# Optimization experiments

Measured on AMD Instinct MI355X. Metric: run time of the kernel, lower is better.

The kernel has to match this reference:

```python
import jax, jax.numpy as jnp
import numpy as np

D, H, M, FF = 1024, 16, 64, 4096
B, N, C = 8, 1024, 256


def setup_inputs() -> dict:
    key = jax.random.key(0)
    it = iter(jax.random.split(key, 24))
    def nrm(shape, s):
        return jax.random.normal(next(it), shape, dtype=jnp.float32) * s
    z = lambda *s: jnp.zeros(s, jnp.float32)
    inp = {
        'point_tokens': nrm((B, N, D), 1.0),
        'context_tokens': nrm((B, C, D), 1.0),
        'inducing': nrm((1, M, D), 0.02),
    }
    for p in ('ti', 'tp'):  # to_induced / to_points MHA
        for w in ('Wq', 'Wk', 'Wv', 'Wo'):
            inp[f'{p}_{w}'] = nrm((D, D), 0.02)
        for b in ('bq', 'bk', 'bv', 'bo'):
            inp[f'{p}_{b}'] = z(D)
    for p in ('iff', 'pff'):  # induced_ff / point_ff: LN + Linear + GELU + Linear
        inp[f'{p}_g'] = jnp.ones(D, jnp.float32); inp[f'{p}_b'] = z(D)
        inp[f'{p}_W1'] = nrm((D, FF), 0.02); inp[f'{p}_b1'] = z(FF)
        inp[f'{p}_W2'] = nrm((FF, D), 0.02); inp[f'{p}_b2'] = z(D)
    inp['ni_g'] = jnp.ones(D, jnp.float32); inp['ni_b'] = z(D)
    inp['np_g'] = jnp.ones(D, jnp.float32); inp['np_b'] = z(D)
    return inp


def layernorm(x, g, b, eps=1e-5):
    mu = x.mean(-1, keepdims=True)
    var = ((x - mu) ** 2).mean(-1, keepdims=True)
    return (x - mu) * jax.lax.rsqrt(var + eps) * g + b


def ffn(x, g, b0, W1, b1, W2, b2):
    h = layernorm(x, g, b0)
    h = jax.nn.gelu(h @ W1 + b1, approximate=False)  # torch nn.GELU default = exact erf
    return h @ W2 + b2


def mha(q, kv, Wq, bq, Wk, bk, Wv, bv, Wo, bo):
    # torch nn.MultiheadAttention semantics (batch_first, dropout=0, need_weights=True)
    Bq, Lq, Dm = q.shape
    Lk = kv.shape[1]
    hd = Dm // H
    Q = (q @ Wq + bq).reshape(Bq, Lq, H, hd)
    K = (kv @ Wk + bk).reshape(Bq, Lk, H, hd)
    V = (kv @ Wv + bv).reshape(Bq, Lk, H, hd)
    scores = jnp.einsum('bqhd,bkhd->bhqk', Q, K) / jnp.sqrt(jnp.float32(hd))
    probs = jax.nn.softmax(scores, axis=-1)
    out = jnp.einsum('bhqk,bkhd->bqhd', probs, V).reshape(Bq, Lq, Dm)
    return out @ Wo + bo, probs.mean(axis=1)  # head-averaged weights (need_weights default)


def reference(point_tokens, context_tokens, inducing,
              ti_Wq, ti_bq, ti_Wk, ti_bk, ti_Wv, ti_bv, ti_Wo, ti_bo,
              tp_Wq, tp_bq, tp_Wk, tp_bk, tp_Wv, tp_bv, tp_Wo, tp_bo,
              iff_g, iff_b, iff_W1, iff_b1, iff_W2, iff_b2,
              pff_g, pff_b, pff_W1, pff_b1, pff_W2, pff_b2,
              ni_g, ni_b, np_g, np_b):
    b = point_tokens.shape[0]
    induced = jnp.broadcast_to(inducing, (b, inducing.shape[1], inducing.shape[2]))
    kv = jnp.concatenate([context_tokens, point_tokens], axis=1)
    ia, _ = mha(induced, kv, ti_Wq, ti_bq, ti_Wk, ti_bk, ti_Wv, ti_bv, ti_Wo, ti_bo)
    induced = layernorm(induced + ia, ni_g, ni_b)
    induced = induced + ffn(induced, iff_g, iff_b, iff_W1, iff_b1, iff_W2, iff_b2)
    kv2 = jnp.concatenate([context_tokens, induced], axis=1)
    pa, w2 = mha(point_tokens, kv2, tp_Wq, tp_bq, tp_Wk, tp_bk, tp_Wv, tp_bv, tp_Wo, tp_bo)
    pts = layernorm(point_tokens + pa, np_g, np_b)
    pts = pts + ffn(pts, pff_g, pff_b, pff_W1, pff_b1, pff_W2, pff_b2)
    probs = jnp.clip(w2, 1e-8, None)
    entropy = (-(probs * jnp.log(probs)).sum(axis=-1)).mean()  # detached side output
    return pts, entropy
```

## Files before the change

kernel.cpp:

```cpp
#include <hip/hip_runtime.h>
#include <hip/hip_bf16.h>
#include <math.h>

typedef unsigned short ushort_t;
typedef __attribute__((ext_vector_type(8))) short short8;
typedef __attribute__((ext_vector_type(4))) float f32x4;

static __device__ __forceinline__ ushort_t f2b(float f){
  union{float f;unsigned u;}a; a.f=f;
  unsigned r = a.u + 0x7fffu + ((a.u>>16)&1u);
  return (ushort_t)(r>>16);
}
static __device__ __forceinline__ float b2f(ushort_t u){
  union{unsigned u;float f;}a; a.u=((unsigned)u)<<16; return a.f;
}

#define GLDS16(g,l) __builtin_amdgcn_global_load_lds((const __attribute__((address_space(1))) void*)(const void*)(g), (__attribute__((address_space(3))) void*)(void*)(l), 16, 0, 0)

template<bool GELU, int RES>
__global__ __launch_bounds__(256)
void gemm_bt(const ushort_t* __restrict__ A, const ushort_t* __restrict__ Bt,
             const float* __restrict__ bias, const void* __restrict__ Res,
             float* __restrict__ Cf, ushort_t* __restrict__ Cb,
             int M, int N, int K, int lda, int ldb, int ldres, int ldcf, int ldcb,
             int nb0,
             long sA0, long sA1, long sB0, long sB1, long sR0, long sR1,
             long sCf0, long sCf1, long sCb0, long sCb1, float scale, int resMask)
{
  const int z = blockIdx.z;
  const int b0 = z % nb0, b1 = z / nb0;
  A  += b0*sA0 + b1*sA1;
  Bt += b0*sB0 + b1*sB1;
  const float* RpF = 0; const ushort_t* RpB = 0;
  if (RES==1) RpF = (const float*)Res + b0*sR0 + b1*sR1;
  if (RES==2) RpB = (const ushort_t*)Res + b0*sR0 + b1*sR1;
  if (Cf) Cf += b0*sCf0 + b1*sCf1;
  if (Cb) Cb += b0*sCb0 + b1*sCb1;

  const int gx = gridDim.x;
  const int nwg = gx * gridDim.y;
  const int orig = blockIdx.y*gx + blockIdx.x;
  const int q8 = nwg >> 3, r8 = nwg & 7;
  const int xcd = orig & 7, ii = orig >> 3;
  const int wg = (xcd < r8 ? xcd*(q8+1) : r8*(q8+1) + (xcd-r8)*q8) + ii;
  const int bm = (wg / gx)*128, bn = (wg % gx)*128;

  __shared__ __align__(16) ushort_t As[2][4096];
  __shared__ __align__(16) ushort_t Bs[2][4096];
  const int tid = threadIdx.x, lane = tid&63, wave = tid>>6;
  const int wr = wave>>1, wc = wave&1;

  f32x4 acc[4][4] = {};

  const int c0 = wave*64 + lane;
  const int c1 = c0 + 256;
  const long rA0 = min(bm + (c0>>2), M-1);
  const long rA1 = min(bm + (c1>>2), M-1);
  const long rB0 = min(bn + (c0>>2), N-1);
  const long rB1 = min(bn + (c1>>2), N-1);
  const ushort_t* pA0 = A + rA0*lda + (c0&3)*8;
  const ushort_t* pA1 = A + rA1*lda + (c1&3)*8;
  const ushort_t* pB0 = Bt + rB0*ldb + (c0&3)*8;
  const ushort_t* pB1 = Bt + rB1*ldb + (c1&3)*8;
  const int ldsOff = wave*512;

  const int lr = lane&15, lk = (lane>>4)*8;

#define STAGE(buf, kt) do { \
    GLDS16(pA0 + (kt), &As[buf][ldsOff]); \
    GLDS16(pA1 + (kt), &As[buf][2048 + ldsOff]); \
    GLDS16(pB0 + (kt), &Bs[buf][ldsOff]); \
    GLDS16(pB1 + (kt), &Bs[buf][2048 + ldsOff]); \
  } while(0)

  STAGE(0, 0);
  __syncthreads();
  int cur = 0;
  for (int kt = 0; kt < K; kt += 32) {
    if (kt + 32 < K) STAGE(cur^1, kt+32);
    short8 af[4], bfv[4];
#pragma unroll
    for (int m=0;m<4;m++) af[m]  = *(const short8*)(&As[cur][(wr*64+m*16+lr)*32 + lk]);
#pragma unroll
    for (int n=0;n<4;n++) bfv[n] = *(const short8*)(&Bs[cur][(wc*64+n*16+lr)*32 + lk]);
#pragma unroll
    for (int m=0;m<4;m++)
#pragma unroll
      for (int n=0;n<4;n++)
        acc[m][n] = __builtin_amdgcn_mfma_f32_16x16x32_bf16(af[m], bfv[n], acc[m][n], 0, 0, 0);
    __syncthreads();
    cur ^= 1;
  }
#undef STAGE

  const int orow = bm + wr*64, ocol = bn + wc*64;
  const int rsub = (lane>>4)*4;
#pragma unroll
  for (int n=0;n<4;n++){
    const int col = ocol + n*16 + lr;
    if (col >= N) continue;
    const float bv = bias ? bias[col] : 0.f;
#pragma unroll
    for (int m=0;m<4;m++){
#pragma unroll
      for (int i=0;i<4;i++){
        const int row = orow + m*16 + rsub + i;
        if (row >= M) continue;
        float v = acc[m][n][i]*scale + bv;
        if (GELU) v = 0.5f*v*(1.f + erff(v*0.70710678118654752f));
        if (RES==1) v += RpF[(long)(row & resMask)*ldres + col];
        if (RES==2) v += b2f(RpB[(long)(row & resMask)*ldres + col]);
        if (Cf) Cf[(long)row*ldcf + col] = v;
        if (Cb) Cb[(long)row*ldcb + col] = f2b(v);
      }
    }
  }
}

template<bool WRITEP>
__global__ __launch_bounds__(256)
void fattn_k(const ushort_t* __restrict__ Qb, const ushort_t* __restrict__ KVb,
             const ushort_t* __restrict__ Vtb, ushort_t* __restrict__ Ob,
             ushort_t* __restrict__ Pb,
             int LK, int ldkv, int qRowsPerB, int oRowsPerB, float scale)
{
  const int z = blockIdx.z, b = z >> 4, h = z & 15;
  const int qt = blockIdx.x;
  const int tid = threadIdx.x, lane = tid & 63, wave = tid >> 6;
  const int lr = lane & 15, g = lane >> 4;

  __shared__ __align__(16) ushort_t Kls[64*68];
  __shared__ __align__(16) ushort_t Vtls[64*68];
  __shared__ __align__(16) ushort_t Pls[64*68];

  const long qrow = (long)b*qRowsPerB + qt*64 + wave*16 + lr;
  const short8 aq0 = *(const short8*)(Qb + qrow*1024 + h*64 + g*8);
  const short8 aq1 = *(const short8*)(Qb + qrow*1024 + h*64 + 32 + g*8);

  const ushort_t* Kbase = KVb + (long)b*LK*ldkv + h*64;
  const ushort_t* Vtbase = Vtb + (long)(b*16+h)*64*LK;

  const int ntiles = LK >> 6;
  const int r0 = tid>>3, d0c = (tid&7)*8;
  const int r1 = r0 + 32;

  float m[4] = {-3e30f,-3e30f,-3e30f,-3e30f};
  float l[4] = {0.f,0.f,0.f,0.f};

  for (int t=0; t<ntiles; ++t){
    __syncthreads();
    { short8 v0 = *(const short8*)(Kbase + (long)(t*64 + r0)*ldkv + d0c);
      short8 v1 = *(const short8*)(Kbase + (long)(t*64 + r1)*ldkv + d0c);
      *(short8*)(Kls + r0*68 + d0c) = v0;
      *(short8*)(Kls + r1*68 + d0c) = v1; }
    __syncthreads();
    f32x4 s[4];
#pragma unroll
    for(int n=0;n<4;n++){
      s[n] = (f32x4){0.f,0.f,0.f,0.f};
      short8 bk0 = *(const short8*)(Kls + (n*16+lr)*68 + g*8);
      short8 bk1 = *(const short8*)(Kls + (n*16+lr)*68 + 32 + g*8);
      s[n] = __builtin_amdgcn_mfma_f32_16x16x32_bf16(aq0, bk0, s[n],0,0,0);
      s[n] = __builtin_amdgcn_mfma_f32_16x16x32_bf16(aq1, bk1, s[n],0,0,0);
    }
#pragma unroll
    for(int i=0;i<4;i++){
      float mx = fmaxf(fmaxf(s[0][i],s[1][i]), fmaxf(s[2][i],s[3][i])) * scale;
#pragma unroll
      for(int o2=1;o2<16;o2<<=1) mx = fmaxf(mx, __shfl_xor(mx,o2));
      float mnew = fmaxf(m[i], mx);
      float sum = __expf(s[0][i]*scale-mnew)+__expf(s[1][i]*scale-mnew)
                + __expf(s[2][i]*scale-mnew)+__expf(s[3][i]*scale-mnew);
#pragma unroll
      for(int o2=1;o2<16;o2<<=1) sum += __shfl_xor(sum,o2);
      l[i] = l[i]*__expf(m[i]-mnew) + sum;
      m[i] = mnew;
    }
  }
  float invl[4];
#pragma unroll
  for(int i=0;i<4;i++) invl[i] = 1.f/l[i];

  f32x4 o[4];
#pragma unroll
  for(int n=0;n<4;n++) o[n] = (f32x4){0.f,0.f,0.f,0.f};

  long pbase = 0;
  if (WRITEP) pbase = ((long)(b*16+h)*1024 + qt*64 + wave*16)*320 + lr;

  for (int t=0; t<ntiles; ++t){
    __syncthreads();
    { short8 v0 = *(const short8*)(Kbase + (long)(t*64 + r0)*ldkv + d0c);
      short8 v1 = *(const short8*)(Kbase + (long)(t*64 + r1)*ldkv + d0c);
      short8 w0 = *(const short8*)(Vtbase + (long)r0*LK + t*64 + d0c);
      short8 w1 = *(const short8*)(Vtbase + (long)r1*LK + t*64 + d0c);
      *(short8*)(Kls + r0*68 + d0c) = v0;
      *(short8*)(Kls + r1*68 + d0c) = v1;
      *(short8*)(Vtls + r0*68 + d0c) = w0;
      *(short8*)(Vtls + r1*68 + d0c) = w1; }
    __syncthreads();
    f32x4 s[4];
#pragma unroll
    for(int n=0;n<4;n++){
      s[n] = (f32x4){0.f,0.f,0.f,0.f};
      short8 bk0 = *(const short8*)(Kls + (n*16+lr)*68 + g*8);
      short8 bk1 = *(const short8*)(Kls + (n*16+lr)*68 + 32 + g*8);
      s[n] = __builtin_amdgcn_mfma_f32_16x16x32_bf16(aq0, bk0, s[n],0,0,0);
      s[n] = __builtin_amdgcn_mfma_f32_16x16x32_bf16(aq1, bk1, s[n],0,0,0);
    }
#pragma unroll
    for(int n=0;n<4;n++){
#pragma unroll
      for(int i=0;i<4;i++){
        float e = __expf(s[n][i]*scale - m[i]);
        Pls[(wave*16 + g*4 + i)*68 + n*16 + lr] = f2b(e);
        if (WRITEP) Pb[pbase + (long)(g*4+i)*320 + t*64 + n*16] = f2b(e*invl[i]);
      }
    }
    short8 pa0 = *(const short8*)(Pls + (wave*16+lr)*68 + g*8);
    short8 pa1 = *(const short8*)(Pls + (wave*16+lr)*68 + 32 + g*8);
#pragma unroll
    for(int nd=0; nd<4; nd++){
      short8 vb0 = *(const short8*)(Vtls + (nd*16+lr)*68 + g*8);
      short8 vb1 = *(const short8*)(Vtls + (nd*16+lr)*68 + 32 + g*8);
      o[nd] = __builtin_amdgcn_mfma_f32_16x16x32_bf16(pa0, vb0, o[nd],0,0,0);
      o[nd] = __builtin_amdgcn_mfma_f32_16x16x32_bf16(pa1, vb1, o[nd],0,0,0);
    }
  }
  const long orow0 = (long)b*oRowsPerB + qt*64 + wave*16 + g*4;
#pragma unroll
  for(int nd=0;nd<4;nd++)
#pragma unroll
    for(int i=0;i<4;i++)
      Ob[(orow0+i)*1024 + h*64 + nd*16 + lr] = f2b(o[nd][i]*invl[i]);
}

__global__ __launch_bounds__(256)
void tcvt_k(const float* __restrict__ src, ushort_t* __restrict__ dst, int R, int C)
{
  __shared__ float t[32][33];
  int c0 = blockIdx.x*32, r0 = blockIdx.y*32;
  int tx = threadIdx.x & 31, ty = threadIdx.x >> 5;
  for (int i=ty;i<32;i+=8){ int r=r0+i, c=c0+tx; t[i][tx] = (r<R && c<C) ? src[(long)r*C + c] : 0.f; }
  __syncthreads();
  for (int i=ty;i<32;i+=8){ int c=c0+i, r=r0+tx; if (c<C && r<R) dst[(long)c*R + r] = f2b(t[tx][i]); }
}

__global__ __launch_bounds__(256)
void cvt_rows_k(const float* __restrict__ src, ushort_t* __restrict__ dst,
                long total, int R, long dstBS, long dstRO)
{
  long e = ((long)blockIdx.x*256 + threadIdx.x)*4;
  if (e >= total) return;
  long rc = e >> 10; int c = (int)(e & 1023);
  int r = (int)(rc % R); long b = rc / R;
  float4 v = *(const float4*)(src + e);
  ushort4 o; o.x=f2b(v.x); o.y=f2b(v.y); o.z=f2b(v.z); o.w=f2b(v.w);
  *(ushort4*)(dst + (b*dstBS + dstRO + r)*1024 + c) = o;
}

__global__ __launch_bounds__(256)
void vtrans_k(const ushort_t* __restrict__ V, ushort_t* __restrict__ Vt,
              int Lk, int ldv, int coloff)
{
  int b = blockIdx.z, h = blockIdx.y, k0 = blockIdx.x*32;
  __shared__ ushort_t t[32][65];
  int tx = threadIdx.x & 63, ty = threadIdx.x >> 6;
  for (int i=ty;i<32;i+=4) t[i][tx] = V[((long)b*Lk + k0 + i)*ldv + coloff + h*64 + tx];
  __syncthreads();
  int kk = threadIdx.x & 31, n0 = threadIdx.x >> 5;
  for (int n=n0;n<64;n+=8) Vt[((long)(b*16+h)*64 + n)*Lk + k0 + kk] = t[kk][n];
}

__global__ __launch_bounds__(256)
void ln2x_k(const float* __restrict__ x,
            const float* __restrict__ g1, const float* __restrict__ b1,
            const float* __restrict__ g2, const float* __restrict__ b2,
            float* __restrict__ y1f, ushort_t* __restrict__ y1b, ushort_t* __restrict__ y2b)
{
  const long row = blockIdx.x;
  int tid = threadIdx.x, lane = tid&63, wave = tid>>6;
  __shared__ float red[8], red2[8];
  float4 v = ((const float4*)(x + row*1024))[tid];
  float s = v.x+v.y+v.z+v.w;
  for (int o=32;o;o>>=1) s += __shfl_down(s,o);
  if (lane==0) red[wave]=s;
  __syncthreads();
  float mean = (red[0]+red[1]+red[2]+red[3])*(1.f/1024.f);
  float d0=v.x-mean, d1=v.y-mean, d2=v.z-mean, d3=v.w-mean;
  float q = d0*d0+d1*d1+d2*d2+d3*d3;
  for (int o=32;o;o>>=1) q += __shfl_down(q,o);
  if (lane==0) red[4+wave]=q;
  __syncthreads();
  float var = (red[4]+red[5]+red[6]+red[7])*(1.f/1024.f);
  float rs = rsqrtf(var+1e-5f);
  float4 gg=((const float4*)g1)[tid], bb=((const float4*)b1)[tid];
  float y0=d0*rs*gg.x+bb.x, y1v=d1*rs*gg.y+bb.y, y2v=d2*rs*gg.z+bb.z, y3=d3*rs*gg.w+bb.w;
  if (y1f) ((float4*)(y1f+row*1024))[tid] = make_float4(y0,y1v,y2v,y3);
  if (y1b){ ushort4 o4; o4.x=f2b(y0); o4.y=f2b(y1v); o4.z=f2b(y2v); o4.w=f2b(y3);
            ((ushort4*)(y1b+row*1024))[tid]=o4; }
  float s2 = y0+y1v+y2v+y3;
  for (int o=32;o;o>>=1) s2 += __shfl_down(s2,o);
  if (lane==0) red2[wave]=s2;
  __syncthreads();
  float mean2 = (red2[0]+red2[1]+red2[2]+red2[3])*(1.f/1024.f);
  float e0=y0-mean2,e1=y1v-mean2,e2=y2v-mean2,e3=y3-mean2;
  float q2 = e0*e0+e1*e1+e2*e2+e3*e3;
  for (int o=32;o;o>>=1) q2 += __shfl_down(q2,o);
  if (lane==0) red2[4+wave]=q2;
  __syncthreads();
  float var2 = (red2[4]+red2[5]+red2[6]+red2[7])*(1.f/1024.f);
  float rs2 = rsqrtf(var2+1e-5f);
  float4 g2v=((const float4*)g2)[tid], b2v=((const float4*)b2)[tid];
  ushort4 o4;
  o4.x=f2b(e0*rs2*g2v.x+b2v.x); o4.y=f2b(e1*rs2*g2v.y+b2v.y);
  o4.z=f2b(e2*rs2*g2v.z+b2v.z); o4.w=f2b(e3*rs2*g2v.w+b2v.w);
  ((ushort4*)(y2b+row*1024))[tid]=o4;
}

__global__ __launch_bounds__(256)
void w2ent_k(const ushort_t* __restrict__ P, float* __restrict__ rowent)
{
  int wid = (int)((blockIdx.x*256 + threadIdx.x) >> 6);
  int lane = threadIdx.x & 63;
  int b = wid >> 10, q = wid & 1023;
  const ushort_t* base = P + ((long)(b*16)*1024 + q)*320;
  float acc = 0.f;
#pragma unroll
  for (int j=0;j<5;j++){
    int k = j*64 + lane;
    float s = 0.f;
#pragma unroll
    for (int h=0;h<16;h++) s += b2f(base[(long)h*327680 + k]);
    float p = fmaxf(s*(1.f/16.f), 1e-8f);
    acc += p*__logf(p);
  }
  for (int o=32;o;o>>=1) acc += __shfl_down(acc, o);
  if (lane==0) rowent[wid] = acc;
}

__global__ __launch_bounds__(256)
void entfin_k(const float* __restrict__ rowent, float* __restrict__ out)
{
  float s = 0.f;
  for (int i=threadIdx.x;i<8192;i+=256) s += rowent[i];
  __shared__ float red[4];
  for (int o=32;o;o>>=1) s += __shfl_down(s,o);
  if ((threadIdx.x&63)==0) red[threadIdx.x>>6]=s;
  __syncthreads();
  if (threadIdx.x==0) out[0] = -(red[0]+red[1]+red[2]+red[3]) * (1.f/8192.f);
}

__global__ void dbg_k(float* out, float a){ out[0] = -12345.f; out[1] = a; }

static void gemm(hipStream_t s, int mode,
                 const void* A, const void* Bt, const float* bias, const void* Res,
                 void* Cf, void* Cb,
                 int M, int N, int K, int lda, int ldb, int ldres, int ldcf, int ldcb,
                 int nz, int nb0,
                 long sA0, long sA1, long sB0, long sB1, long sR0, long sR1,
                 long sCf0, long sCf1, long sCb0, long sCb1, float scale, int resMask)
{
  dim3 g((N+127)/128, (M+127)/128, nz), b(256,1,1);
#define ARGS (const ushort_t*)A,(const ushort_t*)Bt,bias,Res,(float*)Cf,(ushort_t*)Cb,M,N,K,lda,ldb,ldres,ldcf,ldcb,nb0,sA0,sA1,sB0,sB1,sR0,sR1,sCf0,sCf1,sCb0,sCb1,scale,resMask
  if      (mode == 1) gemm_bt<true ,0><<<g,b,0,s>>>(ARGS);
  else if (mode == 2) gemm_bt<false,1><<<g,b,0,s>>>(ARGS);
  else if (mode == 3) gemm_bt<false,2><<<g,b,0,s>>>(ARGS);
  else                gemm_bt<false,0><<<g,b,0,s>>>(ARGS);
#undef ARGS
}

extern "C" void kernel_launch(void* const* d_in, const int* in_sizes, int n_in,
                              void* d_out, int out_size, void* d_ws, size_t ws_size,
                              hipStream_t stream)
{
  const float* ptsIn = (const float*)d_in[0];
  const float* ctx   = (const float*)d_in[1];
  const float* induc = (const float*)d_in[2];
  const float* tiW[4]={(const float*)d_in[3],(const float*)d_in[4],(const float*)d_in[5],(const float*)d_in[6]};
  const float* tib[4]={(const float*)d_in[7],(const float*)d_in[8],(const float*)d_in[9],(const float*)d_in[10]};
  const float* tpW[4]={(const float*)d_in[11],(const float*)d_in[12],(const float*)d_in[13],(const float*)d_in[14]};
  const float* tpb[4]={(const float*)d_in[15],(const float*)d_in[16],(const float*)d_in[17],(const float*)d_in[18]};
  const float* iff_g=(const float*)d_in[19]; const float* iff_b=(const float*)d_in[20];
  const float* iffW1=(const float*)d_in[21]; const float* iff_b1=(const float*)d_in[22];
  const float* iffW2=(const float*)d_in[23]; const float* iff_b2=(const float*)d_in[24];
  const float* pff_g=(const float*)d_in[25]; const float* pff_b=(const float*)d_in[26];
  const float* pffW1=(const float*)d_in[27]; const float* pff_b1=(const float*)d_in[28];
  const float* pffW2=(const float*)d_in[29]; const float* pff_b2=(const float*)d_in[30];
  const float* ni_g=(const float*)d_in[31]; const float* ni_b=(const float*)d_in[32];
  const float* np_g=(const float*)d_in[33]; const float* np_b=(const float*)d_in[34];
  float* outF = (float*)d_out;

  char* ws = (char*)d_ws;
  size_t off = 0;
  auto alloc = [&](size_t bytes){ off=(off+255)&~(size_t)255; size_t o=off; off+=bytes; return o; };
  auto sub = [&](size_t& pp, size_t bytes){ pp=(pp+255)&~(size_t)255; size_t o=pp; pp+=bytes; return o; };

  size_t o_tiQw  = alloc(1024L*1024*2);
  size_t o_tiKVw = alloc(2048L*1024*2);
  size_t o_tiOw  = alloc(1024L*1024*2);
  size_t o_tpQw  = alloc(1024L*1024*2);
  size_t o_tpKVw = alloc(2048L*1024*2);
  size_t o_tpOw  = alloc(1024L*1024*2);
  size_t o_iffW1t = alloc(4096L*1024*2);
  size_t o_iffW2t = alloc(4096L*1024*2);
  size_t o_pffW1t = alloc(4096L*1024*2);
  size_t o_pffW2t = alloc(4096L*1024*2);
  size_t o_bti  = alloc(2048*4);
  size_t o_btp  = alloc(2048*4);
  size_t o_indb = alloc(64L*1024*2);
  size_t o_kv   = alloc(10240L*1024*2);
  size_t o_kv2  = alloc(2560L*1024*2);
  size_t o_rowent = alloc(8192*4);
  off=(off+255)&~(size_t)255;
  size_t arena = off;

  size_t p = arena;
  size_t o_Qti     = sub(p, 64L*1024*2);
  size_t o_KVti    = sub(p, 10240L*2048*2);
  size_t o_Vtti    = sub(p, 8192L*1280*2);
  size_t o_attnOti = sub(p, 512L*1024*2);
  size_t o_t1      = sub(p, 512L*1024*4);
  size_t o_ind1    = sub(p, 512L*1024*4);
  size_t o_h0i     = sub(p, 512L*1024*2);
  size_t o_h1i     = sub(p, 512L*4096*2);
  size_t need1 = p;
  p = arena;
  size_t o_attnOtp = sub(p, 8192L*1024*2);
  size_t shared = p;
  size_t o_Qtp  = sub(p, 8192L*1024*2);
  size_t o_KVtp = sub(p, 2560L*2048*2);
  size_t o_Vttp = sub(p, 8192L*320*2);
  size_t o_P    = sub(p, 8L*16*1024*320*2);
  size_t need3 = p;
  p = shared;
  size_t o_t2   = sub(p, 8192L*1024*4);
  size_t o_pts1 = sub(p, 8192L*1024*2);
  size_t o_h0p  = sub(p, 8192L*1024*2);
  size_t o_h1p  = sub(p, 8192L*4096*2);
  size_t need4 = p;

  size_t need = need1;
  if (need3>need) need=need3;
  if (need4>need) need=need4;
  if (need > ws_size){ dbg_k<<<1,1,0,stream>>>(outF, (float)(need>>20)); return; }

#define WP(o) ((void*)(ws + (o)))
#define BP(o) ((ushort_t*)(ws + (o)))
#define FP(o) ((float*)(ws + (o)))
  const long Z0[10] = {0,0,0,0,0,0,0,0,0,0};

  tcvt_k<<<dim3(32,32),256,0,stream>>>(tiW[0], BP(o_tiQw), 1024, 1024);
  tcvt_k<<<dim3(32,32),256,0,stream>>>(tiW[1], BP(o_tiKVw), 1024, 1024);
  tcvt_k<<<dim3(32,32),256,0,stream>>>(tiW[2], BP(o_tiKVw) + 1024L*1024, 1024, 1024);
  tcvt_k<<<dim3(32,32),256,0,stream>>>(tiW[3], BP(o_tiOw), 1024, 1024);
  tcvt_k<<<dim3(32,32),256,0,stream>>>(tpW[0], BP(o_tpQw), 1024, 1024);
  tcvt_k<<<dim3(32,32),256,0,stream>>>(tpW[1], BP(o_tpKVw), 1024, 1024);
  tcvt_k<<<dim3(32,32),256,0,stream>>>(tpW[2], BP(o_tpKVw) + 1024L*1024, 1024, 1024);
  tcvt_k<<<dim3(32,32),256,0,stream>>>(tpW[3], BP(o_tpOw), 1024, 1024);
  tcvt_k<<<dim3(128,32),256,0,stream>>>(iffW1, BP(o_iffW1t), 1024, 4096);
  tcvt_k<<<dim3(32,128),256,0,stream>>>(iffW2, BP(o_iffW2t), 4096, 1024);
  tcvt_k<<<dim3(128,32),256,0,stream>>>(pffW1, BP(o_pffW1t), 1024, 4096);
  tcvt_k<<<dim3(32,128),256,0,stream>>>(pffW2, BP(o_pffW2t), 4096, 1024);
  hipMemcpyAsync(WP(o_bti), (const void*)tib[1], 1024*4, hipMemcpyDeviceToDevice, stream);
  hipMemcpyAsync((void*)(ws+o_bti+1024*4), (const void*)tib[2], 1024*4, hipMemcpyDeviceToDevice, stream);
  hipMemcpyAsync(WP(o_btp), (const void*)tpb[1], 1024*4, hipMemcpyDeviceToDevice, stream);
  hipMemcpyAsync((void*)(ws+o_btp+1024*4), (const void*)tpb[2], 1024*4, hipMemcpyDeviceToDevice, stream);

  cvt_rows_k<<<2048,256,0,stream>>>(ctx,   BP(o_kv),  8L*256*1024, 256, 1280, 0);
  cvt_rows_k<<<8192,256,0,stream>>>(ptsIn, BP(o_kv),  8L*1024*1024, 1024, 1280, 256);
  cvt_rows_k<<<64,256,0,stream>>>(induc,   BP(o_indb), 64L*1024, 64, 64, 0);
  cvt_rows_k<<<2048,256,0,stream>>>(ctx,   BP(o_kv2), 8L*256*1024, 256, 320, 0);

  gemm(stream,0, WP(o_indb), WP(o_tiQw), tib[0], 0, 0, WP(o_Qti),
       64,1024,1024, 1024,1024,0,0,1024, 1,1, 0,0,0,0,0,0,0,0,0,0, 1.f,-1);
  gemm(stream,0, WP(o_kv), WP(o_tiKVw), FP(o_bti), 0, 0, WP(o_KVti),
       10240,2048,1024, 1024,1024,0,0,2048, 1,1, 0,0,0,0,0,0,0,0,0,0, 1.f,-1);
  vtrans_k<<<dim3(40,16,8),256,0,stream>>>(BP(o_KVti), BP(o_Vtti), 1280, 2048, 1024);
  fattn_k<false><<<dim3(1,1,128),256,0,stream>>>(BP(o_Qti), BP(o_KVti), BP(o_Vtti),
       BP(o_attnOti), (ushort_t*)0, 1280, 2048, 0, 64, 0.125f);
  gemm(stream,2, WP(o_attnOti), WP(o_tiOw), tib[3], (const void*)induc, WP(o_t1), 0,
       512,1024,1024, 1024,1024,1024,1024,0, 1,1, 0,0,0,0,0,0,0,0,0,0, 1.f,63);
  ln2x_k<<<512,256,0,stream>>>(FP(o_t1), ni_g, ni_b, iff_g, iff_b, FP(o_ind1), 0, BP(o_h0i));
  gemm(stream,1, WP(o_h0i), WP(o_iffW1t), iff_b1, 0, 0, WP(o_h1i),
       512,4096,1024, 1024,1024,0,0,4096, 1,1, 0,0,0,0,0,0,0,0,0,0, 1.f,-1);
  gemm(stream,2, WP(o_h1i), WP(o_iffW2t), iff_b2, WP(o_ind1), 0, BP(o_kv2) + 262144,
       64,1024,4096, 4096,4096,1024,0,1024, 8,8,
       262144,0, 0,0, 65536,0, 0,0, 327680,0, 1.f,-1);

  gemm(stream,0, BP(o_kv) + 262144, WP(o_tpQw), tpb[0], 0, 0, WP(o_Qtp),
       1024,1024,1024, 1024,1024,0,0,1024, 8,8,
       1310720,0, 0,0, 0,0, 0,0, 1048576,0, 1.f,-1);
  gemm(stream,0, WP(o_kv2), WP(o_tpKVw), FP(o_btp), 0, 0, WP(o_KVtp),
       2560,2048,1024, 1024,1024,0,0,2048, 1,1, 0,0,0,0,0,0,0,0,0,0, 1.f,-1);
  vtrans_k<<<dim3(10,16,8),256,0,stream>>>(BP(o_KVtp), BP(o_Vttp), 320, 2048, 1024);
  fattn_k<true><<<dim3(16,1,128),256,0,stream>>>(BP(o_Qtp), BP(o_KVtp), BP(o_Vttp),
       BP(o_attnOtp), BP(o_P), 320, 2048, 1024, 1024, 0.125f);
  w2ent_k<<<2048,256,0,stream>>>(BP(o_P), FP(o_rowent));
  entfin_k<<<1,256,0,stream>>>(FP(o_rowent), outF + (out_size-1));
  gemm(stream,2, WP(o_attnOtp), WP(o_tpOw), tpb[3], (const void*)ptsIn, WP(o_t2), 0,
       8192,1024,1024, 1024,1024,1024,1024,0, 1,1, 0,0,0,0,0,0,0,0,0,0, 1.f,-1);
  ln2x_k<<<8192,256,0,stream>>>(FP(o_t2), np_g, np_b, pff_g, pff_b, 0, BP(o_pts1), BP(o_h0p));
  gemm(stream,1, WP(o_h0p), WP(o_pffW1t), pff_b1, 0, 0, WP(o_h1p),
       8192,4096,1024, 1024,1024,0,0,4096, 1,1, 0,0,0,0,0,0,0,0,0,0, 1.f,-1);
  gemm(stream,3, WP(o_h1p), WP(o_pffW2t), pff_b2, WP(o_pts1), outF, 0,
       8192,1024,4096, 4096,4096,1024,1024,0, 1,1, 0,0,0,0,0,0,0,0,0,0, 1.f,-1);

  (void)Z0;
#undef WP
#undef BP
#undef FP
}
```

Before: 927.9 us.

## Single-buffer GEMM, grouped block swizzle, tanh-style GELU, reordered epilogue

The GEMM kernel drops LDS double-buffering in favour of a single buffer with two barriers per K-step, which halves shared memory and may allow more resident workgroups, but the global loads no longer overlap the MFMA work. Workgroups are remapped into groups of 8 row-tiles after the XCD swizzle to improve L2 reuse. Exact erf GELU is replaced by a sigmoid-based tanh approximation that is cheaper but numerically different. The epilogue is reordered so bias values are loaded once and the row loop is outermost.

New measurement: 924.9 us. About the same (-0.3%).

```diff
diff --git a/kernel.cpp b/kernel.cpp
--- a/kernel.cpp
+++ b/kernel.cpp
@@ -14,8 +14,27 @@
 static __device__ __forceinline__ float b2f(ushort_t u){
   union{unsigned u;float f;}a; a.u=((unsigned)u)<<16; return a.f;
 }
+static __device__ __forceinline__ float gelu_f(float v){
+  float u = 1.595769122f*v*(1.f + 0.044715f*v*v);
+  return v / (1.f + __expf(-u));
+}
 
 #define GLDS16(g,l) __builtin_amdgcn_global_load_lds((const __attribute__((address_space(1))) void*)(const void*)(g), (__attribute__((address_space(3))) void*)(void*)(l), 16, 0, 0)
+
+static __device__ __forceinline__ void block_map(int GM, int& by, int& bx)
+{
+  const int gx = gridDim.x, gy = gridDim.y;
+  const int nwg = gx*gy;
+  const int orig = blockIdx.y*gx + blockIdx.x;
+  const int q8 = nwg >> 3, r8 = nwg & 7;
+  const int xcd = orig & 7, ii = orig >> 3;
+  const int wg = (xcd < r8 ? xcd*(q8+1) : r8*(q8+1) + (xcd-r8)*q8) + ii;
+  const int stripe = wg / (GM*gx);
+  const int rem = wg - stripe*(GM*gx);
+  const int gmEff = min(GM, gy - stripe*GM);
+  bx = rem / gmEff;
+  by = stripe*GM + (rem - bx*gmEff);
+}
 
 template<bool GELU, int RES>
 __global__ __launch_bounds__(256)
@@ -37,16 +56,11 @@
   if (Cf) Cf += b0*sCf0 + b1*sCf1;
   if (Cb) Cb += b0*sCb0 + b1*sCb1;
 
-  const int gx = gridDim.x;
-  const int nwg = gx * gridDim.y;
-  const int orig = blockIdx.y*gx + blockIdx.x;
-  const int q8 = nwg >> 3, r8 = nwg & 7;
-  const int xcd = orig & 7, ii = orig >> 3;
-  const int wg = (xcd < r8 ? xcd*(q8+1) : r8*(q8+1) + (xcd-r8)*q8) + ii;
-  const int bm = (wg / gx)*128, bn = (wg % gx)*128;
-
-  __shared__ __align__(16) ushort_t As[2][4096];
-  __shared__ __align__(16) ushort_t Bs[2][4096];
+  int by, bx; block_map(8, by, bx);
+  const int bm = by*128, bn = bx*128;
+
+  __shared__ __align__(16) ushort_t As[4096];
+  __shared__ __align__(16) ushort_t Bs[4096];
   const int tid = threadIdx.x, lane = tid&63, wave = tid>>6;
   const int wr = wave>>1, wc = wave&1;
 
@@ -66,48 +80,45 @@
 
   const int lr = lane&15, lk = (lane>>4)*8;
 
-#define STAGE(buf, kt) do { \
-    GLDS16(pA0 + (kt), &As[buf][ldsOff]); \
-    GLDS16(pA1 + (kt), &As[buf][2048 + ldsOff]); \
-    GLDS16(pB0 + (kt), &Bs[buf][ldsOff]); \
-    GLDS16(pB1 + (kt), &Bs[buf][2048 + ldsOff]); \
-  } while(0)
-
-  STAGE(0, 0);
-  __syncthreads();
-  int cur = 0;
   for (int kt = 0; kt < K; kt += 32) {
-    if (kt + 32 < K) STAGE(cur^1, kt+32);
+    __syncthreads();
+    GLDS16(pA0 + kt, As + ldsOff);
+    GLDS16(pA1 + kt, As + 2048 + ldsOff);
+    GLDS16(pB0 + kt, Bs + ldsOff);
+    GLDS16(pB1 + kt, Bs + 2048 + ldsOff);
+    __syncthreads();
     short8 af[4], bfv[4];
 #pragma unroll
-    for (int m=0;m<4;m++) af[m]  = *(const short8*)(&As[cur][(wr*64+m*16+lr)*32 + lk]);
-#pragma unroll
-    for (int n=0;n<4;n++) bfv[n] = *(const short8*)(&Bs[cur][(wc*64+n*16+lr)*32 + lk]);
+    for (int m=0;m<4;m++) af[m]  = *(const short8*)(As + (wr*64+m*16+lr)*32 + lk);
+#pragma unroll
+    for (int n=0;n<4;n++) bfv[n] = *(const short8*)(Bs + (wc*64+n*16+lr)*32 + lk);
 #pragma unroll
     for (int m=0;m<4;m++)
 #pragma unroll
       for (int n=0;n<4;n++)
         acc[m][n] = __builtin_amdgcn_mfma_f32_16x16x32_bf16(af[m], bfv[n], acc[m][n], 0, 0, 0);
-    __syncthreads();
-    cur ^= 1;
   }
-#undef STAGE
 
   const int orow = bm + wr*64, ocol = bn + wc*64;
   const int rsub = (lane>>4)*4;
+  float bv[4];
 #pragma unroll
   for (int n=0;n<4;n++){
     const int col = ocol + n*16 + lr;
-    if (col >= N) continue;
-    const float bv = bias ? bias[col] : 0.f;
-#pragma unroll
-    for (int m=0;m<4;m++){
-#pragma unroll
-      for (int i=0;i<4;i++){
-        const int row = orow + m*16 + rsub + i;
-        if (row >= M) continue;
-        float v = acc[m][n][i]*scale + bv;
-        if (GELU) v = 0.5f*v*(1.f + erff(v*0.70710678118654752f));
+    bv[n] = (bias && col < N) ? bias[col] : 0.f;
+  }
+#pragma unroll
+  for (int m=0;m<4;m++){
+#pragma unroll
+    for (int i=0;i<4;i++){
+      const int row = orow + m*16 + rsub + i;
+      if (row >= M) continue;
+#pragma unroll
+      for (int n=0;n<4;n++){
+        const int col = ocol + n*16 + lr;
+        if (col >= N) continue;
+        float v = acc[m][n][i]*scale + bv[n];
+        if (GELU) v = gelu_f(v);
         if (RES==1) v += RpF[(long)(row & resMask)*ldres + col];
         if (RES==2) v += b2f(RpB[(long)(row & resMask)*ldres + col]);
         if (Cf) Cf[(long)row*ldcf + col] = v;
@@ -448,7 +459,6 @@
 #define WP(o) ((void*)(ws + (o)))
 #define BP(o) ((ushort_t*)(ws + (o)))
 #define FP(o) ((float*)(ws + (o)))
-  const long Z0[10] = {0,0,0,0,0,0,0,0,0,0};
 
   tcvt_k<<<dim3(32,32),256,0,stream>>>(tiW[0], BP(o_tiQw), 1024, 1024);
   tcvt_k<<<dim3(32,32),256,0,stream>>>(tiW[1], BP(o_tiKVw), 1024, 1024);
@@ -506,7 +516,6 @@
   gemm(stream,3, WP(o_h1p), WP(o_pffW2t), pff_b2, WP(o_pts1), outF, 0,
        8192,1024,4096, 4096,4096,1024,1024,0, 1,1, 0,0,0,0,0,0,0,0,0,0, 1.f,-1);
 
-  (void)Z0;
 #undef WP
 #undef BP
 #undef FP
```
